# Kernel optimization log

Hardware: AMD Instinct MI355X
Metric: run time of the kernel (lower is better)

The kernel has to match this reference:

```python
import jax, jax.numpy as jnp
import numpy as np

B, N, C = 8, 1024, 768
NUM_HEADS = 12
HEAD_DIM = C // NUM_HEADS  # 64
WS = 32                    # window_size[0] == window_size[1] == H == W
REL_DIM = 2 * WS - 1       # 63


def setup_inputs() -> dict:
    key = jax.random.key(0)
    ks = jax.random.split(key, 7)
    x = jax.random.normal(ks[0], (B, N, C), dtype=jnp.float32)
    qkv_w = jax.random.normal(ks[1], (3 * C, C), dtype=jnp.float32) * 0.02
    qkv_b = jnp.zeros((3 * C,), dtype=jnp.float32)
    proj_w = jax.random.normal(ks[2], (C, C), dtype=jnp.float32) * 0.02
    proj_b = jnp.zeros((C,), dtype=jnp.float32)
    rel_pos_h = jax.random.normal(ks[3], (REL_DIM, HEAD_DIM), dtype=jnp.float32) * 0.02
    rel_pos_w = jax.random.normal(ks[4], (REL_DIM, HEAD_DIM), dtype=jnp.float32) * 0.02
    return {
        "x": x,
        "qkv_w": qkv_w,
        "qkv_b": qkv_b,
        "proj_w": proj_w,
        "proj_b": proj_b,
        "rel_pos_h": rel_pos_h,
        "rel_pos_w": rel_pos_w,
        "H": WS,
        "W": WS,
    }


def reference(x, qkv_w, qkv_b, proj_w, proj_b, rel_pos_h, rel_pos_w, H, W):
    B_, N_, C_ = x.shape
    heads = NUM_HEADS
    hd = C_ // heads
    scale = hd ** -0.5

    # qkv projection: (B, N, 3, heads, hd) -> (3, B, heads, N, hd)
    qkv = (x @ qkv_w.T + qkv_b).reshape(B_, N_, 3, heads, hd).transpose(2, 0, 3, 1, 4)
    q, k, v = qkv[0], qkv[1], qkv[2]
    q = q * scale

    # raw scores (B, heads, N, N)
    attn = jnp.einsum('bhqd,bhkd->bhqk', q, k)

    # decomposed relative position bias (q_shape == k_shape -> ratios are 1.0)
    dist_h = jnp.arange(H)[:, None] - jnp.arange(H)[None, :] + (H - 1)
    dist_w = jnp.arange(W)[:, None] - jnp.arange(W)[None, :] + (W - 1)
    Rh = rel_pos_h[dist_h]  # (H, H, hd)
    Rw = rel_pos_w[dist_w]  # (W, W, hd)

    r_q = q.reshape(B_, heads, H, W, hd)
    rel_h = jnp.einsum('byhwc,hkc->byhwk', r_q, Rh)  # (B, heads, H, W, k_h)
    rel_w = jnp.einsum('byhwc,wkc->byhwk', r_q, Rw)  # (B, heads, H, W, k_w)

    attn = (attn.reshape(B_, heads, H, W, H, W)
            + rel_h[:, :, :, :, :, None]
            + rel_w[:, :, :, :, None, :]).reshape(B_, heads, N_, N_)

    attn = jax.nn.softmax(attn, axis=-1)
    out = jnp.einsum('bhqk,bhkd->bhqd', attn, v)
    out = out.transpose(0, 2, 1, 3).reshape(B_, N_, heads * hd)
    return out @ proj_w.T + proj_b
```

## Files before the change

kernel.cpp:

```cpp
#include <hip/hip_runtime.h>
#include <cstddef>

typedef short s4v __attribute__((ext_vector_type(4)));
typedef short s8v __attribute__((ext_vector_type(8)));
typedef float f4v __attribute__((ext_vector_type(4)));

__device__ __forceinline__ unsigned short f2bf(float f) {
    union { float f; unsigned u; } v; v.f = f;
    unsigned r = v.u + 0x7fff + ((v.u >> 16) & 1);
    return (unsigned short)(r >> 16);
}
__device__ __forceinline__ float bf2f(unsigned short u) {
    union { unsigned u; float f; } v; v.u = ((unsigned)u) << 16;
    return v.f;
}

__device__ __forceinline__ void gl_lds16(const void* g, void* l) {
    __builtin_amdgcn_global_load_lds(
        (const __attribute__((address_space(1))) void*)g,
        (__attribute__((address_space(3))) void*)l, 16, 0, 0);
}

#define QSC   0.18033688011112043f
#define EOFF  23.082320654223414f

__global__ __launch_bounds__(256) void to_bf16_all(
    const float* __restrict__ x, const float* __restrict__ qw,
    const float* __restrict__ pw, unsigned short* __restrict__ xd,
    unsigned short* __restrict__ qd, unsigned short* __restrict__ pd)
{
    int i = blockIdx.x * 256 + threadIdx.x;
    const float* s; unsigned short* d; int j;
    if (i < 786432)       { s = x;  d = xd; j = i; }
    else if (i < 1007616) { s = qw; d = qd; j = i - 786432; }
    else                  { s = pw; d = pd; j = i - 1007616; }
    float4 f0 = ((const float4*)s)[j * 2];
    float4 f1 = ((const float4*)s)[j * 2 + 1];
    uint4 pk;
    pk.x = (unsigned)f2bf(f0.x) | ((unsigned)f2bf(f0.y) << 16);
    pk.y = (unsigned)f2bf(f0.z) | ((unsigned)f2bf(f0.w) << 16);
    pk.z = (unsigned)f2bf(f1.x) | ((unsigned)f2bf(f1.y) << 16);
    pk.w = (unsigned)f2bf(f1.z) | ((unsigned)f2bf(f1.w) << 16);
    ((uint4*)d)[j] = pk;
}

__global__ __launch_bounds__(256) void qkv_gemm_mfma(
    const unsigned short* __restrict__ A, const unsigned short* __restrict__ W,
    const float* __restrict__ bias,
    unsigned short* __restrict__ qb, unsigned short* __restrict__ kb,
    unsigned short* __restrict__ vt)
{
    __shared__ __align__(16) unsigned short As[2][128 * 32];
    __shared__ __align__(16) unsigned short Bs[2][128 * 32];
    const int t     = threadIdx.x;
    const int lin   = blockIdx.x;
    const int xcd   = lin & 7;
    const int sq    = lin >> 3;
    const int br    = (xcd << 3) + (sq & 7);
    const int bc    = sq >> 3;
    const int wv    = t >> 6;
    const int lane  = t & 63;
    const int col16 = lane & 15;
    const int quad  = lane >> 4;
    const int w4    = lane >> 2;
    const int k8    = (lane & 3) << 3;
    const int mw    = wv >> 1, nw = wv & 1;

    const unsigned short* Ag = A + (size_t)(br * 128 + (wv << 5) + w4) * 768 + k8;
    const unsigned short* Wg = W + (size_t)(bc * 128 + (wv << 5) + w4) * 768 + k8;
    const int wo = (wv << 5) * 32;

    f4v acc[4][4];
#pragma unroll
    for (int mt = 0; mt < 4; ++mt)
#pragma unroll
        for (int nt = 0; nt < 4; ++nt) {
            acc[mt][nt][0] = 0.f; acc[mt][nt][1] = 0.f;
            acc[mt][nt][2] = 0.f; acc[mt][nt][3] = 0.f;
        }

    gl_lds16(Ag,            &As[0][wo]);
    gl_lds16(Ag + 16 * 768, &As[0][wo + 16 * 32]);
    gl_lds16(Wg,            &Bs[0][wo]);
    gl_lds16(Wg + 16 * 768, &Bs[0][wo + 16 * 32]);

    for (int k0 = 0; k0 < 768; k0 += 32) {
        __syncthreads();
        const int cur = (k0 >> 5) & 1;
        if (k0 < 736) {
            unsigned short* An = &As[cur ^ 1][wo];
            unsigned short* Bn = &Bs[cur ^ 1][wo];
            gl_lds16(Ag + k0 + 32,            An);
            gl_lds16(Ag + k0 + 32 + 16 * 768, An + 16 * 32);
            gl_lds16(Wg + k0 + 32,            Bn);
            gl_lds16(Wg + k0 + 32 + 16 * 768, Bn + 16 * 32);
        }
        const unsigned short* Ab = As[cur];
        const unsigned short* Bb = Bs[cur];

        s8v a[4], b[4];
#pragma unroll
        for (int mt = 0; mt < 4; ++mt)
            a[mt] = *(const s8v*)&Ab[(mw * 64 + mt * 16 + col16) * 32 + quad * 8];
#pragma unroll
        for (int nt = 0; nt < 4; ++nt)
            b[nt] = *(const s8v*)&Bb[(nw * 64 + nt * 16 + col16) * 32 + quad * 8];
#pragma unroll
        for (int mt = 0; mt < 4; ++mt)
#pragma unroll
            for (int nt = 0; nt < 4; ++nt)
                acc[mt][nt] = __builtin_amdgcn_mfma_f32_16x16x32_bf16(
                    a[mt], b[nt], acc[mt][nt], 0, 0, 0);
    }

    const int which = bc / 6;
    const int cb    = (bc % 6) * 128 + nw * 64;
    const int m0    = br * 128 + mw * 64 + quad * 4;
    if (which == 2) {
#pragma unroll
        for (int nt = 0; nt < 4; ++nt) {
            int c    = cb + nt * 16 + col16;
            int head = c >> 6, d = c & 63;
            float bv = bias[1536 + c];
#pragma unroll
            for (int mt = 0; mt < 4; ++mt) {
                int mb  = m0 + mt * 16;
                int bbk = mb >> 10, tok = mb & 1023;
                uint2 pk;
                pk.x = (unsigned)f2bf(acc[mt][nt][0] + bv)
                     | ((unsigned)f2bf(acc[mt][nt][1] + bv) << 16);
                pk.y = (unsigned)f2bf(acc[mt][nt][2] + bv)
                     | ((unsigned)f2bf(acc[mt][nt][3] + bv) << 16);
                *(uint2*)&vt[((size_t)(bbk * 12 + head)) * 65536 + (size_t)d * 1024 + tok] = pk;
            }
        }
    } else {
        const float sc = (which == 0) ? QSC : 1.0f;
        unsigned short* dst = (which == 0) ? qb : kb;
#pragma unroll
        for (int nt = 0; nt < 4; ++nt) {
            int c    = cb + nt * 16 + col16;
            int head = c >> 6, d = c & 63;
            float bv = bias[which * 768 + c];
#pragma unroll
            for (int mt = 0; mt < 4; ++mt) {
#pragma unroll
                for (int i = 0; i < 4; ++i) {
                    int m   = m0 + mt * 16 + i;
                    int bbk = m >> 10, tok = m & 1023;
                    dst[(((size_t)(bbk * 12 + head) << 10) + tok) * 64 + d] =
                        f2bf((acc[mt][nt][i] + bv) * sc);
                }
            }
        }
    }
}

__global__ __launch_bounds__(256) void proj_gemm_mfma(
    const unsigned short* __restrict__ A, const unsigned short* __restrict__ W,
    const float* __restrict__ bias, float* __restrict__ Out)
{
    __shared__ __align__(16) unsigned short As[2][128 * 32];
    __shared__ __align__(16) unsigned short Bs[2][128 * 32];
    const int t     = threadIdx.x;
    const int lin   = blockIdx.x;
    const int xcd   = lin & 7;
    const int sq    = lin >> 3;
    const int br    = (xcd << 3) + (sq & 7);
    const int bc    = sq >> 3;
    const int wv    = t >> 6;
    const int lane  = t & 63;
    const int col16 = lane & 15;
    const int quad  = lane >> 4;
    const int w4    = lane >> 2;
    const int k8    = (lane & 3) << 3;
    const int mw    = wv >> 1, nw = wv & 1;

    const unsigned short* Ag = A + (size_t)(br * 128 + (wv << 5) + w4) * 768 + k8;
    const unsigned short* Wg = W + (size_t)(bc * 128 + (wv << 5) + w4) * 768 + k8;
    const int wo = (wv << 5) * 32;

    f4v acc[4][4];
#pragma unroll
    for (int mt = 0; mt < 4; ++mt)
#pragma unroll
        for (int nt = 0; nt < 4; ++nt) {
            acc[mt][nt][0] = 0.f; acc[mt][nt][1] = 0.f;
            acc[mt][nt][2] = 0.f; acc[mt][nt][3] = 0.f;
        }

    gl_lds16(Ag,            &As[0][wo]);
    gl_lds16(Ag + 16 * 768, &As[0][wo + 16 * 32]);
    gl_lds16(Wg,            &Bs[0][wo]);
    gl_lds16(Wg + 16 * 768, &Bs[0][wo + 16 * 32]);

    for (int k0 = 0; k0 < 768; k0 += 32) {
        __syncthreads();
        const int cur = (k0 >> 5) & 1;
        if (k0 < 736) {
            unsigned short* An = &As[cur ^ 1][wo];
            unsigned short* Bn = &Bs[cur ^ 1][wo];
            gl_lds16(Ag + k0 + 32,            An);
            gl_lds16(Ag + k0 + 32 + 16 * 768, An + 16 * 32);
            gl_lds16(Wg + k0 + 32,            Bn);
            gl_lds16(Wg + k0 + 32 + 16 * 768, Bn + 16 * 32);
        }
        const unsigned short* Ab = As[cur];
        const unsigned short* Bb = Bs[cur];

        s8v a[4], b[4];
#pragma unroll
        for (int mt = 0; mt < 4; ++mt)
            a[mt] = *(const s8v*)&Ab[(mw * 64 + mt * 16 + col16) * 32 + quad * 8];
#pragma unroll
        for (int nt = 0; nt < 4; ++nt)
            b[nt] = *(const s8v*)&Bb[(nw * 64 + nt * 16 + col16) * 32 + quad * 8];
#pragma unroll
        for (int mt = 0; mt < 4; ++mt)
#pragma unroll
            for (int nt = 0; nt < 4; ++nt)
                acc[mt][nt] = __builtin_amdgcn_mfma_f32_16x16x32_bf16(
                    a[mt], b[nt], acc[mt][nt], 0, 0, 0);
    }

    const int m0 = br * 128 + mw * 64 + quad * 4;
#pragma unroll
    for (int nt = 0; nt < 4; ++nt) {
        int c    = bc * 128 + nw * 64 + nt * 16 + col16;
        float bv = bias[c];
#pragma unroll
        for (int mt = 0; mt < 4; ++mt) {
#pragma unroll
            for (int i = 0; i < 4; ++i) {
                int m = m0 + mt * 16 + i;
                Out[(size_t)m * 768 + c] = acc[mt][nt][i] + bv;
            }
        }
    }
}

__global__ __launch_bounds__(256) void bias_prep_mfma(
    const unsigned short* __restrict__ Q, const float* __restrict__ Rh,
    const float* __restrict__ Rw, unsigned short* __restrict__ qhb,
    unsigned short* __restrict__ qwb)
{
    __shared__ __align__(16) char smem[36864];
    unsigned short (*Qs)[72]  = (unsigned short (*)[72])smem;
    unsigned short (*Rs)[72]  = (unsigned short (*)[72])(smem + 18432);
    unsigned short (*Wsm)[72] = (unsigned short (*)[72])(smem + 27648);
    float (*G)[66]            = (float (*)[66])smem;

    const int t    = threadIdx.x;
    const int tc8  = blockIdx.x;
    const int bh   = blockIdx.y;
    const int tok0 = tc8 << 7;

    for (int id = t; id < 1024; id += 256) {
        int row = id >> 3, g8 = (id & 7) << 3;
        *(uint4*)&Qs[row][g8] =
            *(const uint4*)(Q + ((size_t)bh * 1024 + tok0 + row) * 64 + g8);
    }
    for (int id = t; id < 512; id += 256) {
        int row = id >> 3, g8 = (id & 7) << 3;
        unsigned short* dh = &Rs[row][g8];
        unsigned short* dw = &Wsm[row][g8];
        if (row < 63) {
            const float* sh = Rh + row * 64 + g8;
            const float* sw = Rw + row * 64 + g8;
            float4 a = *(const float4*)sh; float4 b = *(const float4*)(sh + 4);
            float4 c = *(const float4*)sw; float4 d = *(const float4*)(sw + 4);
            dh[0] = f2bf(a.x); dh[1] = f2bf(a.y); dh[2] = f2bf(a.z); dh[3] = f2bf(a.w);
            dh[4] = f2bf(b.x); dh[5] = f2bf(b.y); dh[6] = f2bf(b.z); dh[7] = f2bf(b.w);
            dw[0] = f2bf(c.x); dw[1] = f2bf(c.y); dw[2] = f2bf(c.z); dw[3] = f2bf(c.w);
            dw[4] = f2bf(d.x); dw[5] = f2bf(d.y); dw[6] = f2bf(d.z); dw[7] = f2bf(d.w);
        } else {
#pragma unroll
            for (int j = 0; j < 8; ++j) { dh[j] = 0; dw[j] = 0; }
        }
    }
    __syncthreads();

    const int wv    = t >> 6;
    const int lane  = t & 63;
    const int col16 = lane & 15;
    const int quad  = lane >> 4;
    const int r0    = wv << 5;

    s8v qa[2][2], rb[4][2], wb[4][2];
#pragma unroll
    for (int mt = 0; mt < 2; ++mt)
#pragma unroll
        for (int kc = 0; kc < 2; ++kc)
            qa[mt][kc] = *(const s8v*)&Qs[r0 + mt * 16 + col16][kc * 32 + quad * 8];
#pragma unroll
    for (int nt = 0; nt < 4; ++nt)
#pragma unroll
        for (int kc = 0; kc < 2; ++kc) {
            rb[nt][kc] = *(const s8v*)&Rs[nt * 16 + col16][kc * 32 + quad * 8];
            wb[nt][kc] = *(const s8v*)&Wsm[nt * 16 + col16][kc * 32 + quad * 8];
        }

    f4v ah[2][4], aw[2][4];
#pragma unroll
    for (int mt = 0; mt < 2; ++mt)
#pragma unroll
        for (int nt = 0; nt < 4; ++nt) {
            f4v z; z[0] = 0.f; z[1] = 0.f; z[2] = 0.f; z[3] = 0.f;
            ah[mt][nt] = z; aw[mt][nt] = z;
        }
#pragma unroll
    for (int mt = 0; mt < 2; ++mt)
#pragma unroll
        for (int nt = 0; nt < 4; ++nt) {
            ah[mt][nt] = __builtin_amdgcn_mfma_f32_16x16x32_bf16(qa[mt][0], rb[nt][0], ah[mt][nt], 0, 0, 0);
            ah[mt][nt] = __builtin_amdgcn_mfma_f32_16x16x32_bf16(qa[mt][1], rb[nt][1], ah[mt][nt], 0, 0, 0);
            aw[mt][nt] = __builtin_amdgcn_mfma_f32_16x16x32_bf16(qa[mt][0], wb[nt][0], aw[mt][nt], 0, 0, 0);
            aw[mt][nt] = __builtin_amdgcn_mfma_f32_16x16x32_bf16(qa[mt][1], wb[nt][1], aw[mt][nt], 0, 0, 0);
        }
    __syncthreads();

#pragma unroll
    for (int mt = 0; mt < 2; ++mt)
#pragma unroll
        for (int nt = 0; nt < 4; ++nt)
#pragma unroll
            for (int i = 0; i < 4; ++i)
                G[r0 + mt * 16 + quad * 4 + i][nt * 16 + col16] = ah[mt][nt][i];
    __syncthreads();
    for (int id = t; id < 2048; id += 256) {
        int tok = id >> 4, c2 = (id & 15) << 1;
        int i_img = (tc8 << 2) + (tok >> 5);
        float g0 = G[tok][i_img - c2 + 31];
        float g1 = G[tok][i_img - c2 + 30];
        unsigned pk = (unsigned)f2bf(g0) | ((unsigned)f2bf(g1) << 16);
        *(unsigned*)&qhb[(((size_t)bh << 10) + tok0 + tok) * 32 + c2] = pk;
    }
    __syncthreads();

#pragma unroll
    for (int mt = 0; mt < 2; ++mt)
#pragma unroll
        for (int nt = 0; nt < 4; ++nt)
#pragma unroll
            for (int i = 0; i < 4; ++i)
                G[r0 + mt * 16 + quad * 4 + i][nt * 16 + col16] = aw[mt][nt][i];
    __syncthreads();
    for (int id = t; id < 2048; id += 256) {
        int tok = id >> 4, c2 = (id & 15) << 1;
        int j = tok & 31;
        float g0 = G[tok][j - c2 + 31];
        float g1 = G[tok][j - c2 + 30];
        unsigned pk = (unsigned)f2bf(g0) | ((unsigned)f2bf(g1) << 16);
        *(unsigned*)&qwb[(((size_t)bh << 10) + tok0 + tok) * 32 + c2] = pk;
    }
}

__global__ __launch_bounds__(256, 4) void attn_mfma(
    const unsigned short* __restrict__ Q, const unsigned short* __restrict__ K,
    const unsigned short* __restrict__ Vt,
    const unsigned short* __restrict__ qhb, const unsigned short* __restrict__ qwb,
    unsigned short* __restrict__ Out)
{
    const int t  = threadIdx.x;
    const int id  = blockIdx.x;
    const int xcd = id & 7;
    const int wq  = id >> 3;
    const int bh  = xcd * 12 + (wq % 12);
    const int qt2 = wq / 12;
    const int b   = bh / 12;
    const int h   = bh - b * 12;
    const int q0  = qt2 << 6;

    __shared__ __align__(16) unsigned short Ks[64 * 72];
    __shared__ __align__(16) unsigned short Vs[64 * 72];
    __shared__ float qh_s[64][33];

    const unsigned short* Kp = K  + (size_t)bh * 65536;
    const unsigned short* Vp = Vt + (size_t)bh * 65536;

    {
        const unsigned* qhp = (const unsigned*)(qhb + ((size_t)bh * 1024 + q0) * 32);
        for (int i2 = t; i2 < 1024; i2 += 256) {
            int row = i2 >> 4, c2 = (i2 & 15) << 1;
            unsigned ph = qhp[i2];
            qh_s[row][c2]     = bf2f((unsigned short)(ph & 0xffff)) - EOFF;
            qh_s[row][c2 + 1] = bf2f((unsigned short)(ph >> 16))    - EOFF;
        }
    }

    const int wv = t >> 6;
    const int lane = t & 63;
    const int c  = lane & 15;
    const int qd = lane >> 4;

    s8v qf0, qf1;
    float uw[8];
    {
        const size_t row = (size_t)bh * 1024 + q0 + (wv << 4) + c;
        const unsigned short* qp = Q + row * 64 + qd * 8;
        qf0 = *(const s8v*)qp;
        qf1 = *(const s8v*)(qp + 32);
        s8v w8 = *(const s8v*)(qwb + row * 32 + qd * 8);
#pragma unroll
        for (int j = 0; j < 8; ++j) uw[j] = bf2f((unsigned short)w8[j]);
    }

    const int e0 = t * 8, e1 = t * 8 + 2048;
    const int g0 = e0 >> 6, g1 = e1 >> 6, s0 = e0 & 63, s1 = e1 & 63;
    const int L0 = (g0 & 32) | ((g0 & 4) << 2) | ((g0 & 24) >> 1) | (g0 & 3);
    const int L1 = (g1 & 32) | ((g1 & 4) << 2) | ((g1 & 24) >> 1) | (g1 & 3);
    {
        uint4 pk0 = *(const uint4*)(Kp + e0);
        uint4 pk1 = *(const uint4*)(Kp + e1);
        uint4 pv0 = *(const uint4*)(Vp + (size_t)g0 * 1024 + s0);
        uint4 pv1 = *(const uint4*)(Vp + (size_t)g1 * 1024 + s1);
        *(uint4*)&Ks[L0 * 72 + s0] = pk0;
        *(uint4*)&Ks[L1 * 72 + s1] = pk1;
        *(uint4*)&Vs[g0 * 72 + s0] = pv0;
        *(uint4*)&Vs[g1 * 72 + s1] = pv1;
    }
    __syncthreads();

    f4v o[4];
#pragma unroll
    for (int dt = 0; dt < 4; ++dt) { o[dt][0] = 0.f; o[dt][1] = 0.f; o[dt][2] = 0.f; o[dt][3] = 0.f; }
    float lp = 0.f;

    for (int kt = 0; kt < 16; ++kt) {
        uint4 pk0, pk1, pv0, pv1;
        if (kt < 15) {
            const int k0n = (kt + 1) << 6;
            pk0 = *(const uint4*)(Kp + (size_t)k0n * 64 + e0);
            pk1 = *(const uint4*)(Kp + (size_t)k0n * 64 + e1);
            pv0 = *(const uint4*)(Vp + (size_t)g0 * 1024 + k0n + s0);
            pv1 = *(const uint4*)(Vp + (size_t)g1 * 1024 + k0n + s1);
        }

        f4v sc[4];
#pragma unroll
        for (int T = 0; T < 4; ++T) {
            s8v lo = *(const s8v*)&Ks[(T * 16 + c) * 72 + qd * 8];
            s8v hi = *(const s8v*)&Ks[(T * 16 + c) * 72 + 32 + qd * 8];
            f4v z; z[0] = 0.f; z[1] = 0.f; z[2] = 0.f; z[3] = 0.f;
            z = __builtin_amdgcn_mfma_f32_16x16x32_bf16(lo, qf0, z, 0, 0, 0);
            z = __builtin_amdgcn_mfma_f32_16x16x32_bf16(hi, qf1, z, 0, 0, 0);
            sc[T] = z;
        }

        const float qhv0 = qh_s[(wv << 4) + c][(kt << 1)];
        const float qhv1 = qh_s[(wv << 4) + c][(kt << 1) + 1];

        s8v pa0, pa1;
#pragma unroll
        for (int j = 0; j < 4; ++j) {
            float pe = __builtin_amdgcn_exp2f(sc[0][j] + qhv0 + uw[j]);
            lp += pe; pa0[j] = (short)f2bf(pe);
        }
#pragma unroll
        for (int j = 0; j < 4; ++j) {
            float pe = __builtin_amdgcn_exp2f(sc[1][j] + qhv0 + uw[4 + j]);
            lp += pe; pa0[4 + j] = (short)f2bf(pe);
        }
#pragma unroll
        for (int j = 0; j < 4; ++j) {
            float pe = __builtin_amdgcn_exp2f(sc[2][j] + qhv1 + uw[j]);
            lp += pe; pa1[j] = (short)f2bf(pe);
        }
#pragma unroll
        for (int j = 0; j < 4; ++j) {
            float pe = __builtin_amdgcn_exp2f(sc[3][j] + qhv1 + uw[4 + j]);
            lp += pe; pa1[4 + j] = (short)f2bf(pe);
        }

#pragma unroll
        for (int dt = 0; dt < 4; ++dt) {
            s8v vlo = *(const s8v*)&Vs[(dt * 16 + c) * 72 + qd * 8];
            s8v vhi = *(const s8v*)&Vs[(dt * 16 + c) * 72 + 32 + qd * 8];
            o[dt] = __builtin_amdgcn_mfma_f32_16x16x32_bf16(pa0, vlo, o[dt], 0, 0, 0);
            o[dt] = __builtin_amdgcn_mfma_f32_16x16x32_bf16(pa1, vhi, o[dt], 0, 0, 0);
        }

        __syncthreads();
        if (kt < 15) {
            *(uint4*)&Ks[L0 * 72 + s0] = pk0;
            *(uint4*)&Ks[L1 * 72 + s1] = pk1;
            *(uint4*)&Vs[g0 * 72 + s0] = pv0;
            *(uint4*)&Vs[g1 * 72 + s1] = pv1;
        }
        __syncthreads();
    }

    lp += __shfl_xor(lp, 16);
    lp += __shfl_xor(lp, 32);

#pragma unroll
    for (int i = 0; i < 4; ++i) {
        float inv = 1.f / __shfl(lp, (qd << 2) + i);
        int qr = q0 + (wv << 4) + (qd << 2) + i;
        unsigned short* dst = Out + ((size_t)b * 1024 + qr) * 768 + h * 64;
#pragma unroll
        for (int dt = 0; dt < 4; ++dt)
            dst[dt * 16 + c] = f2bf(o[dt][i] * inv);
    }
}

extern "C" void kernel_launch(void* const* d_in, const int* in_sizes, int n_in,
                              void* d_out, int out_size, void* d_ws, size_t ws_size,
                              hipStream_t stream) {
    const float* x      = (const float*)d_in[0];
    const float* qkv_w  = (const float*)d_in[1];
    const float* qkv_b  = (const float*)d_in[2];
    const float* proj_w = (const float*)d_in[3];
    const float* proj_b = (const float*)d_in[4];
    const float* rel_h  = (const float*)d_in[5];
    const float* rel_w  = (const float*)d_in[6];
    float* out = (float*)d_out;

    char* ws = (char*)d_ws;
    unsigned short* qbuf  = (unsigned short*)(ws);
    unsigned short* kbuf  = (unsigned short*)(ws + 12582912);
    unsigned short* vtbuf = (unsigned short*)(ws + 25165824);
    unsigned short* xab   = (unsigned short*)(ws + 37748736);
    unsigned short* wqb   = (unsigned short*)(ws + 50331648);
    unsigned short* wpb   = (unsigned short*)(ws + 53870592);
    unsigned short* qhb   = (unsigned short*)(ws + 55050240);
    unsigned short* qwb   = (unsigned short*)(ws + 61341696);

    to_bf16_all<<<4224, 256, 0, stream>>>(x, qkv_w, proj_w, xab, wqb, wpb);
    qkv_gemm_mfma<<<1152, 256, 0, stream>>>(xab, wqb, qkv_b, qbuf, kbuf, vtbuf);
    bias_prep_mfma<<<dim3(8, 96), 256, 0, stream>>>(qbuf, rel_h, rel_w, qhb, qwb);
    attn_mfma<<<1536, 256, 0, stream>>>(qbuf, kbuf, vtbuf, qhb, qwb, xab);
    proj_gemm_mfma<<<384, 256, 0, stream>>>(xab, wpb, proj_b, out);
}
```

Before: 226.6 us.

## Enlarge GEMM tiles to 256x128 with 8-wave blocks for QKV and projection

Both the QKV and output-projection GEMMs now use 512-thread blocks, each covering a 256-row by 128-column tile instead of 128x128. The loading pattern and block-index swizzle are adjusted to fit: each wave loads 32 A rows and 16 B rows. The aim is to reuse the B (weight) tile across more rows and halve the block count, cutting global/LDS traffic per output. In exchange it doubles LDS for A, and for the projection only 192 blocks are launched, which may underfill the GPU's compute units.

```diff
diff --git a/kernel.cpp b/kernel.cpp
--- a/kernel.cpp
+++ b/kernel.cpp
@@ -44,31 +44,33 @@
     ((uint4*)d)[j] = pk;
 }
 
-__global__ __launch_bounds__(256) void qkv_gemm_mfma(
+__global__ __launch_bounds__(512) void qkv_gemm_mfma(
     const unsigned short* __restrict__ A, const unsigned short* __restrict__ W,
     const float* __restrict__ bias,
     unsigned short* __restrict__ qb, unsigned short* __restrict__ kb,
     unsigned short* __restrict__ vt)
 {
-    __shared__ __align__(16) unsigned short As[2][128 * 32];
+    __shared__ __align__(16) unsigned short As[2][256 * 32];
     __shared__ __align__(16) unsigned short Bs[2][128 * 32];
     const int t     = threadIdx.x;
     const int lin   = blockIdx.x;
     const int xcd   = lin & 7;
     const int sq    = lin >> 3;
-    const int br    = (xcd << 3) + (sq & 7);
-    const int bc    = sq >> 3;
+    const int br    = (xcd << 2) + (sq & 3);
+    const int bc    = sq >> 2;
     const int wv    = t >> 6;
     const int lane  = t & 63;
     const int col16 = lane & 15;
     const int quad  = lane >> 4;
     const int w4    = lane >> 2;
     const int k8    = (lane & 3) << 3;
-    const int mw    = wv >> 1, nw = wv & 1;
-
-    const unsigned short* Ag = A + (size_t)(br * 128 + (wv << 5) + w4) * 768 + k8;
-    const unsigned short* Wg = W + (size_t)(bc * 128 + (wv << 5) + w4) * 768 + k8;
-    const int wo = (wv << 5) * 32;
+    const int mw    = wv >> 1;
+    const int nw    = wv & 1;
+
+    const unsigned short* Ag = A + (size_t)(br * 256 + (wv << 5) + w4) * 768 + k8;
+    const unsigned short* Wg = W + (size_t)(bc * 128 + (wv << 4) + w4) * 768 + k8;
+    const int woA = (wv << 5) * 32;
+    const int woB = (wv << 4) * 32;
 
     f4v acc[4][4];
 #pragma unroll
@@ -79,21 +81,17 @@
             acc[mt][nt][2] = 0.f; acc[mt][nt][3] = 0.f;
         }
 
-    gl_lds16(Ag,            &As[0][wo]);
-    gl_lds16(Ag + 16 * 768, &As[0][wo + 16 * 32]);
-    gl_lds16(Wg,            &Bs[0][wo]);
-    gl_lds16(Wg + 16 * 768, &Bs[0][wo + 16 * 32]);
+    gl_lds16(Ag,            &As[0][woA]);
+    gl_lds16(Ag + 16 * 768, &As[0][woA + 16 * 32]);
+    gl_lds16(Wg,            &Bs[0][woB]);
 
     for (int k0 = 0; k0 < 768; k0 += 32) {
         __syncthreads();
         const int cur = (k0 >> 5) & 1;
         if (k0 < 736) {
-            unsigned short* An = &As[cur ^ 1][wo];
-            unsigned short* Bn = &Bs[cur ^ 1][wo];
-            gl_lds16(Ag + k0 + 32,            An);
-            gl_lds16(Ag + k0 + 32 + 16 * 768, An + 16 * 32);
-            gl_lds16(Wg + k0 + 32,            Bn);
-            gl_lds16(Wg + k0 + 32 + 16 * 768, Bn + 16 * 32);
+            gl_lds16(Ag + k0 + 32,            &As[cur ^ 1][woA]);
+            gl_lds16(Ag + k0 + 32 + 16 * 768, &As[cur ^ 1][woA + 16 * 32]);
+            gl_lds16(Wg + k0 + 32,            &Bs[cur ^ 1][woB]);
         }
         const unsigned short* Ab = As[cur];
         const unsigned short* Bb = Bs[cur];
@@ -115,7 +113,7 @@
 
     const int which = bc / 6;
     const int cb    = (bc % 6) * 128 + nw * 64;
-    const int m0    = br * 128 + mw * 64 + quad * 4;
+    const int m0    = br * 256 + mw * 64 + quad * 4;
     if (which == 2) {
 #pragma unroll
         for (int nt = 0; nt < 4; ++nt) {
@@ -156,18 +154,18 @@
     }
 }
 
-__global__ __launch_bounds__(256) void proj_gemm_mfma(
+__global__ __launch_bounds__(512) void proj_gemm_mfma(
     const unsigned short* __restrict__ A, const unsigned short* __restrict__ W,
     const float* __restrict__ bias, float* __restrict__ Out)
 {
-    __shared__ __align__(16) unsigned short As[2][128 * 32];
+    __shared__ __align__(16) unsigned short As[2][256 * 32];
     __shared__ __align__(16) unsigned short Bs[2][128 * 32];
     const int t     = threadIdx.x;
     const int lin   = blockIdx.x;
     const int xcd   = lin & 7;
     const int sq    = lin >> 3;
-    const int br    = (xcd << 3) + (sq & 7);
-    const int bc    = sq >> 3;
+    const int br    = (xcd << 2) + (sq & 3);
+    const int bc    = sq >> 2;
     const int wv    = t >> 6;
     const int lane  = t & 63;
     const int col16 = lane & 15;
@@ -176,9 +174,10 @@
     const int k8    = (lane & 3) << 3;
     const int mw    = wv >> 1, nw = wv & 1;
 
-    const unsigned short* Ag = A + (size_t)(br * 128 + (wv << 5) + w4) * 768 + k8;
-    const unsigned short* Wg = W + (size_t)(bc * 128 + (wv << 5) + w4) * 768 + k8;
-    const int wo = (wv << 5) * 32;
+    const unsigned short* Ag = A + (size_t)(br * 256 + (wv << 5) + w4) * 768 + k8;
+    const unsigned short* Wg = W + (size_t)(bc * 128 + (wv << 4) + w4) * 768 + k8;
+    const int woA = (wv << 5) * 32;
+    const int woB = (wv << 4) * 32;
 
     f4v acc[4][4];
 #pragma unroll
@@ -189,21 +188,17 @@
             acc[mt][nt][2] = 0.f; acc[mt][nt][3] = 0.f;
         }
 
-    gl_lds16(Ag,            &As[0][wo]);
-    gl_lds16(Ag + 16 * 768, &As[0][wo + 16 * 32]);
-    gl_lds16(Wg,            &Bs[0][wo]);
-    gl_lds16(Wg + 16 * 768, &Bs[0][wo + 16 * 32]);
+    gl_lds16(Ag,            &As[0][woA]);
+    gl_lds16(Ag + 16 * 768, &As[0][woA + 16 * 32]);
+    gl_lds16(Wg,            &Bs[0][woB]);
 
     for (int k0 = 0; k0 < 768; k0 += 32) {
         __syncthreads();
         const int cur = (k0 >> 5) & 1;
         if (k0 < 736) {
-            unsigned short* An = &As[cur ^ 1][wo];
-            unsigned short* Bn = &Bs[cur ^ 1][wo];
-            gl_lds16(Ag + k0 + 32,            An);
-            gl_lds16(Ag + k0 + 32 + 16 * 768, An + 16 * 32);
-            gl_lds16(Wg + k0 + 32,            Bn);
-            gl_lds16(Wg + k0 + 32 + 16 * 768, Bn + 16 * 32);
+            gl_lds16(Ag + k0 + 32,            &As[cur ^ 1][woA]);
+            gl_lds16(Ag + k0 + 32 + 16 * 768, &As[cur ^ 1][woA + 16 * 32]);
+            gl_lds16(Wg + k0 + 32,            &Bs[cur ^ 1][woB]);
         }
         const unsigned short* Ab = As[cur];
         const unsigned short* Bb = Bs[cur];
@@ -223,7 +218,7 @@
                     a[mt], b[nt], acc[mt][nt], 0, 0, 0);
     }
 
-    const int m0 = br * 128 + mw * 64 + quad * 4;
+    const int m0 = br * 256 + mw * 64 + quad * 4;
 #pragma unroll
     for (int nt = 0; nt < 4; ++nt) {
         int c    = bc * 128 + nw * 64 + nt * 16 + col16;
@@ -527,8 +522,8 @@
     unsigned short* qwb   = (unsigned short*)(ws + 61341696);
 
     to_bf16_all<<<4224, 256, 0, stream>>>(x, qkv_w, proj_w, xab, wqb, wpb);
-    qkv_gemm_mfma<<<1152, 256, 0, stream>>>(xab, wqb, qkv_b, qbuf, kbuf, vtbuf);
+    qkv_gemm_mfma<<<576, 512, 0, stream>>>(xab, wqb, qkv_b, qbuf, kbuf, vtbuf);
     bias_prep_mfma<<<dim3(8, 96), 256, 0, stream>>>(qbuf, rel_h, rel_w, qhb, qwb);
     attn_mfma<<<1536, 256, 0, stream>>>(qbuf, kbuf, vtbuf, qhb, qwb, xab);
-    proj_gemm_mfma<<<384, 256, 0, stream>>>(xab, wpb, proj_b, out);
-}
+    proj_gemm_mfma<<<192, 512, 0, stream>>>(xab, wpb, proj_b, out);
+}
```

Result: faster. 215.7 us (-4.8%).
